# Optimization experiments

Measured on AMD Instinct MI355X. Metric: run time of the kernel, lower is better.

The kernel has to match this reference:

```python
import jax, jax.numpy as jnp
import numpy as np

B, D, N = 8, 512, 4096
HEADS, DH = 8, 64
HID = HEADS * DH  # 512
SCALE = DH ** -0.5


def setup_inputs() -> dict:
    key = jax.random.key(0)
    k0, k1, k2, k3 = jax.random.split(key, 4)
    x = jax.random.normal(k0, (B, D, N), dtype=jnp.float32)
    w_qkv = jax.random.normal(k1, (3 * HID, D), dtype=jnp.float32) * 0.02
    w_out = jax.random.normal(k2, (D, HID), dtype=jnp.float32) * 0.02
    b_out = jax.random.normal(k3, (D,), dtype=jnp.float32) * 0.02
    g = jnp.ones((1, D, 1), dtype=jnp.float32)
    return {"x": x, "w_qkv": w_qkv, "w_out": w_out, "b_out": b_out, "g": g}


def reference(x, w_qkv, w_out, b_out, g):
    # 1x1 Conv1d (no bias) == channel matmul: [b, 3*HID, n]
    qkv = jnp.einsum('od,bdn->bon', w_qkv, x)
    q, k, v = jnp.split(qkv, 3, axis=1)
    # b (h c) n -> b h c n
    q = q.reshape(B, HEADS, DH, N)
    k = k.reshape(B, HEADS, DH, N)
    v = v.reshape(B, HEADS, DH, N)
    q = jax.nn.softmax(q, axis=2) * SCALE  # softmax over feature dim d
    k = jax.nn.softmax(k, axis=3)          # softmax over sequence dim n
    context = jnp.einsum('bhdn,bhen->bhde', k, v)   # [b,h,d,e]
    out = jnp.einsum('bhde,bhdn->bhen', context, q)  # [b,h,e,n]
    out = out.reshape(B, HID, N)
    # 1x1 Conv1d with bias
    y = jnp.einsum('oh,bhn->bon', w_out, out) + b_out[None, :, None]
    # RMSNorm: F.normalize(y, dim=1) * g * sqrt(D)
    norm = jnp.sqrt(jnp.sum(y * y, axis=1, keepdims=True))
    y = y / jnp.maximum(norm, 1e-12) * g * jnp.asarray(D, y.dtype) ** 0.5
    return y
```

## Files before the change

kernel.cpp:

```cpp
#include <hip/hip_runtime.h>
#include <math.h>

#define B 8
#define D 512
#define N 4096
#define HEADS 8
#define DH 64
#define HID 512
#define O3 1536
#define KDIM 512
#define SCALE 0.125f
#define SQRT_D 22.62741699796952f

typedef __attribute__((ext_vector_type(4))) float f32x4;
typedef __attribute__((ext_vector_type(8))) short bf16x8;

static __device__ __forceinline__ unsigned short f2bf(float f) {
    unsigned int u = __float_as_uint(f);
    unsigned int r = (u + 0x7fffu + ((u >> 16) & 1u)) >> 16;
    return (unsigned short)r;
}

static __device__ __forceinline__ float bf2f(unsigned short u) {
    return __uint_as_float((unsigned int)u << 16);
}

static __device__ __forceinline__ void gload_lds16(const void* g, void* l) {
    __builtin_amdgcn_global_load_lds(
        (const __attribute__((address_space(1))) unsigned int*)g,
        (__attribute__((address_space(3))) unsigned int*)l, 16, 0, 0);
}

__global__ __launch_bounds__(256) void prep(const float* __restrict__ x,
                                            unsigned short* __restrict__ xT,
                                            const float* __restrict__ w,
                                            unsigned short* __restrict__ wb) {
    if (blockIdx.z == B) {
        int i = ((blockIdx.y * 96 + blockIdx.x) * 256 + threadIdx.x) * 4;
        float4 v = *(const float4*)(w + i);
        __align__(8) unsigned short o[4] = {f2bf(v.x), f2bf(v.y), f2bf(v.z), f2bf(v.w)};
        *(uint2*)(wb + i) = *(const uint2*)o;
        return;
    }
    if (blockIdx.x >= 64) return;
    __shared__ float tile[64][65];
    const int n0 = blockIdx.x * 64, d0 = blockIdx.y * 64, b = blockIdx.z;
    const float* xb = x + (size_t)b * D * N;
    unsigned short* xTb = xT + (size_t)b * N * KDIM;
    const int t = threadIdx.x;
    const int r = t >> 4, c4 = (t & 15) * 4;
#pragma unroll
    for (int i = 0; i < 4; ++i) {
        int row = r + i * 16;
        float4 v = *(const float4*)(xb + (size_t)(d0 + row) * N + n0 + c4);
        tile[row][c4 + 0] = v.x;
        tile[row][c4 + 1] = v.y;
        tile[row][c4 + 2] = v.z;
        tile[row][c4 + 3] = v.w;
    }
    __syncthreads();
#pragma unroll
    for (int pass = 0; pass < 2; ++pass) {
        int orow = (t >> 3) + pass * 32;
        int oc = (t & 7) * 8;
        __align__(16) unsigned short o[8];
#pragma unroll
        for (int e = 0; e < 8; ++e) o[e] = f2bf(tile[oc + e][orow]);
        *(uint4*)(xTb + (size_t)(n0 + orow) * KDIM + d0 + oc) = *(const uint4*)o;
    }
}

#define STAGE_H(PTR, REGION, TILE0, KT, H)                                         \
    _Pragma("unroll") for (int sub = 0; sub < 2; ++sub)                            \
        gload_lds16(PTR + (size_t)((TILE0) + (H) * 128 + spr[sub]) * KDIM          \
                        + (KT) * 64 + scoff[sub],                                  \
                    lds + (REGION) + ((KT) & 1) * 32768 + (H) * 16384              \
                        + sub * 8192 + t * 16);

#define PHASE_A(MG, KS)                                                            \
    _Pragma("unroll") for (int j = 0; j < 4; ++j)                                  \
        afr[j] = *(const bf16x8*)(lds + rbuf + arb + ((MG) * 4 + j) * 2048 + xa[KS]);

#define PHASE_B(KS)                                                               \
    _Pragma("unroll") for (int nf = 0; nf < 4; ++nf)                               \
        bfr[nf] = *(const bf16x8*)(lds + 65536 + rbuf + brb + nf * 2048 + xa[KS]);

#define PHASE_MMA(MG)                                                              \
    asm volatile("s_waitcnt lgkmcnt(0)" ::: "memory");                             \
    __builtin_amdgcn_sched_barrier(0);                                             \
    __builtin_amdgcn_s_setprio(1);                                                 \
    _Pragma("unroll") for (int j = 0; j < 4; ++j)                                  \
        _Pragma("unroll") for (int nf = 0; nf < 4; ++nf)                           \
            acc[(MG) * 4 + j][nf] = __builtin_amdgcn_mfma_f32_16x16x32_bf16(       \
                afr[j], bfr[nf], acc[(MG) * 4 + j][nf], 0, 0, 0);                  \
    __builtin_amdgcn_s_setprio(0);

#define PBAR __builtin_amdgcn_s_barrier();

#define GEMM256_CORE(A_PTR, BT_PTR)                                                \
    __shared__ __align__(16) char lds[131072];                                     \
    const int t = threadIdx.x;                                                     \
    const int lane = t & 63;                                                       \
    const int wid = t >> 6;                                                        \
    const int wm = wid >> 2, wn = wid & 3;                                         \
    int spr[2], scoff[2];                                                          \
    _Pragma("unroll") for (int sub = 0; sub < 2; ++sub) {                          \
        int p = sub * 8192 + t * 16;                                               \
        spr[sub] = p >> 7;                                                         \
        int spc = (p >> 4) & 7;                                                    \
        scoff[sub] = (spc ^ (spr[sub] & 7)) * 8;                                   \
    }                                                                              \
    int xa[2];                                                                     \
    _Pragma("unroll") for (int ks = 0; ks < 2; ++ks)                               \
        xa[ks] = ((ks * 4 + (lane >> 4)) ^ (lane & 7)) << 4;                       \
    const int arb = (wm * 128 + (lane & 15)) * 128;                                \
    const int brb = (wn * 64 + (lane & 15)) * 128;                                 \
    f32x4 acc[8][4] = {};                                                          \
    bf16x8 afr[4], bfr[4];                                                         \
    STAGE_H(A_PTR, 0, row0, 0, 0)                                                  \
    STAGE_H(A_PTR, 0, row0, 0, 1)                                                  \
    STAGE_H(BT_PTR, 65536, col0, 0, 0)                                             \
    STAGE_H(BT_PTR, 65536, col0, 0, 1)                                             \
    for (int kt = 0; kt < 8; ++kt) {                                               \
        const int rbuf = (kt & 1) * 32768;                                         \
        if (kt < 7) {                                                              \
            STAGE_H(A_PTR, 0, row0, kt + 1, 0)                                     \
            STAGE_H(A_PTR, 0, row0, kt + 1, 1)                                     \
            STAGE_H(BT_PTR, 65536, col0, kt + 1, 0)                                \
            STAGE_H(BT_PTR, 65536, col0, kt + 1, 1)                                \
            asm volatile("s_waitcnt vmcnt(8)" ::: "memory");                       \
        } else {                                                                   \
            asm volatile("s_waitcnt vmcnt(0)" ::: "memory");                       \
        }                                                                          \
        __builtin_amdgcn_s_barrier();                                              \
        __builtin_amdgcn_sched_barrier(0);                                         \
        PHASE_A(0, 0) PHASE_B(0) PHASE_MMA(0) PBAR                                 \
        PHASE_A(1, 0) PHASE_MMA(1) PBAR                                            \
        PHASE_A(0, 1) PHASE_B(1) PHASE_MMA(0) PBAR                                 \
        PHASE_A(1, 1) PHASE_MMA(1) PBAR                                            \
    }

__global__ __launch_bounds__(512, 2) void gemm_qkv(const unsigned short* __restrict__ Aw,
                                                   const unsigned short* __restrict__ BTall,
                                                   unsigned short* __restrict__ qT,
                                                   unsigned short* __restrict__ kvall) {
    const int b = blockIdx.z;
    const unsigned short* A = Aw;
    const unsigned short* BT = BTall + (size_t)b * N * KDIM;
    const int row0 = blockIdx.y * 256;
    const int col0 = blockIdx.x * 256;
    GEMM256_CORE(A, BT)

    const int g = lane >> 4;
    if (blockIdx.y < 2) {
#pragma unroll
        for (int g2 = 0; g2 < 2; ++g2) {
            const int h = blockIdx.y * 4 + wm * 2 + g2;
#pragma unroll
            for (int nf = 0; nf < 4; ++nf) {
                float mx = -1e30f;
#pragma unroll
                for (int j = 0; j < 4; ++j)
#pragma unroll
                    for (int r = 0; r < 4; ++r) mx = fmaxf(mx, acc[g2 * 4 + j][nf][r]);
                mx = fmaxf(mx, __shfl_xor(mx, 16));
                mx = fmaxf(mx, __shfl_xor(mx, 32));
                float e[16];
                float s = 0.f;
#pragma unroll
                for (int j = 0; j < 4; ++j)
#pragma unroll
                    for (int r = 0; r < 4; ++r) {
                        e[j * 4 + r] = __expf(acc[g2 * 4 + j][nf][r] - mx);
                        s += e[j * 4 + r];
                    }
                s += __shfl_xor(s, 16);
                s += __shfl_xor(s, 32);
                float rs = SCALE / s;
                int n = col0 + wn * 64 + nf * 16 + (lane & 15);
                unsigned short* dst = qT + ((size_t)b * N + n) * KDIM + h * 64 + g * 4;
#pragma unroll
                for (int j = 0; j < 4; ++j) {
                    __align__(8) unsigned short o4[4] = {
                        f2bf(e[j * 4 + 0] * rs), f2bf(e[j * 4 + 1] * rs),
                        f2bf(e[j * 4 + 2] * rs), f2bf(e[j * 4 + 3] * rs)};
                    *(uint2*)(dst + j * 16) = *(const uint2*)o4;
                }
            }
        }
    } else {
        unsigned short* C = kvall + (size_t)b * 1024 * N;
        const int rbase = row0 - 512 + wm * 128;
#pragma unroll
        for (int mf = 0; mf < 8; ++mf) {
            int row_b = rbase + mf * 16 + g * 4;
#pragma unroll
            for (int nf = 0; nf < 4; ++nf) {
                int col = col0 + wn * 64 + nf * 16 + (lane & 15);
#pragma unroll
                for (int r = 0; r < 4; ++r)
                    C[(size_t)(row_b + r) * N + col] = f2bf(acc[mf][nf][r]);
            }
        }
    }
}

__global__ __launch_bounds__(256) void context_mfma3(const unsigned short* __restrict__ kvb,
                                                     float* __restrict__ ctx,
                                                     float* __restrict__ ksum) {
    const int ch = blockIdx.x, h = blockIdx.y, b = blockIdx.z;
    const int K0 = ch * 512;
    const unsigned short* kbase = kvb + ((size_t)b * 1024 + h * DH) * (size_t)N + K0;
    const unsigned short* vbase = kvb + ((size_t)b * 1024 + 512 + h * DH) * (size_t)N + K0;

    __shared__ __align__(16) unsigned short Ks[64 * 64];
    __shared__ __align__(16) unsigned short Vs[64 * 64];

    const int t = threadIdx.x;
    const int lane = t & 63;
    const int wv = t >> 6;

    const int kr = t >> 2;
    const int kc = (t & 3) * 16;
    const int kchunk0 = kc >> 3;
    const int kdst0 = kr * 128 + (((kchunk0 + 0) ^ (kr & 7)) << 4);
    const int kdst1 = kr * 128 + (((kchunk0 + 1) ^ (kr & 7)) << 4);

    int vrow[2], vcoff[2];
#pragma unroll
    for (int i = 0; i < 2; ++i) {
        int p = i * 4096 + t * 16;
        int pr = p >> 7;
        int pc = (p >> 4) & 7;
        vrow[i] = pr;
        vcoff[i] = (pc ^ (pr & 7)) * 8;
    }

    const int ar = wv * 16 + (lane & 15);
    int aoff[2], boff[4][2];
#pragma unroll
    for (int s = 0; s < 2; ++s) {
        int chunk = s * 4 + (lane >> 4);
        aoff[s] = ar * 128 + ((chunk ^ (ar & 7)) << 4);
#pragma unroll
        for (int nf = 0; nf < 4; ++nf) {
            int br = nf * 16 + (lane & 15);
            boff[nf][s] = br * 128 + ((chunk ^ (br & 7)) << 4);
        }
    }

    bf16x8 ones;
#pragma unroll
    for (int j = 0; j < 8; ++j) ones[j] = (short)0x3F80;

    f32x4 acc[4] = {};
    f32x4 accs = {};

    for (int k0 = 0; k0 < 512; k0 += 64) {
#pragma unroll
        for (int i = 0; i < 2; ++i)
            gload_lds16(vbase + (size_t)vrow[i] * N + k0 + vcoff[i],
                        (char*)Vs + i * 4096 + t * 16);
        __align__(16) unsigned short raw[16];
        *(uint4*)raw = *(const uint4*)(kbase + (size_t)kr * N + k0 + kc);
        *(uint4*)(raw + 8) = *(const uint4*)(kbase + (size_t)kr * N + k0 + kc + 8);
        __align__(16) unsigned short o[16];
#pragma unroll
        for (int j = 0; j < 16; ++j) o[j] = f2bf(__expf(bf2f(raw[j])));
        *(uint4*)((char*)Ks + kdst0) = *(const uint4*)o;
        *(uint4*)((char*)Ks + kdst1) = *(const uint4*)(o + 8);
        __syncthreads();

        bf16x8 av[2], bv[4][2];
#pragma unroll
        for (int s = 0; s < 2; ++s) {
            av[s] = *(const bf16x8*)((const char*)Ks + aoff[s]);
#pragma unroll
            for (int nf = 0; nf < 4; ++nf)
                bv[nf][s] = *(const bf16x8*)((const char*)Vs + boff[nf][s]);
        }
#pragma unroll
        for (int s = 0; s < 2; ++s) {
#pragma unroll
            for (int nf = 0; nf < 4; ++nf)
                acc[nf] = __builtin_amdgcn_mfma_f32_16x16x32_bf16(av[s], bv[nf][s], acc[nf], 0, 0, 0);
            accs = __builtin_amdgcn_mfma_f32_16x16x32_bf16(av[s], ones, accs, 0, 0, 0);
        }
        __syncthreads();
    }

    float* cbase = ctx + ((size_t)(b * HEADS + h)) * DH * DH;
    const int drow = wv * 16 + (lane >> 4) * 4;
#pragma unroll
    for (int nf = 0; nf < 4; ++nf) {
        int e = nf * 16 + (lane & 15);
#pragma unroll
        for (int rr = 0; rr < 4; ++rr)
            atomicAdd(&cbase[(drow + rr) * DH + e], acc[nf][rr]);
    }
    if ((lane & 15) == 0) {
#pragma unroll
        for (int rr = 0; rr < 4; ++rr)
            atomicAdd(&ksum[b * 512 + h * DH + drow + rr], accs[rr]);
    }
}

__global__ __launch_bounds__(256) void fold_wout3(const float* __restrict__ w_out,
                                                  const float* __restrict__ ctx,
                                                  const float* __restrict__ ksum,
                                                  unsigned short* __restrict__ w2) {
    const int ot = blockIdx.x, h = blockIdx.y, b = blockIdx.z;
    __shared__ __align__(16) unsigned short As[128 * 64];
    __shared__ __align__(16) unsigned short Bs[64 * 64];
    const int t = threadIdx.x;
    const int lane = t & 63;
    const int wv = t >> 6;

#pragma unroll
    for (int i = 0; i < 8; ++i) {
        int lin = t + i * 256;
        int r = lin >> 4;
        int c4 = (lin & 15) * 4;
        float4 v = *(const float4*)(w_out + (size_t)(ot * 128 + r) * HID + h * 64 + c4);
        __align__(8) unsigned short o4[4] = {f2bf(v.x), f2bf(v.y), f2bf(v.z), f2bf(v.w)};
        int chunk = c4 >> 3;
        int off = (c4 & 7) * 2;
        *(uint2*)((char*)As + r * 128 + ((chunk ^ (r & 7)) << 4) + off) = *(const uint2*)o4;
    }
    const float* cb = ctx + ((size_t)(b * HEADS + h)) * DH * DH;
    const float* ks = ksum + b * 512 + h * 64;
#pragma unroll
    for (int i = 0; i < 4; ++i) {
        int lin = t + i * 256;
        int r = lin >> 4;
        int c4 = (lin & 15) * 4;
        float inv = 1.0f / ks[r];
        float4 v = *(const float4*)(cb + (size_t)r * DH + c4);
        __align__(8) unsigned short o4[4] = {f2bf(v.x * inv), f2bf(v.y * inv),
                                             f2bf(v.z * inv), f2bf(v.w * inv)};
        int chunk = c4 >> 3;
        int off = (c4 & 7) * 2;
        *(uint2*)((char*)Bs + r * 128 + ((chunk ^ (r & 7)) << 4) + off) = *(const uint2*)o4;
    }
    __syncthreads();

    f32x4 acc[2][4] = {};
#pragma unroll
    for (int s = 0; s < 2; ++s) {
        int chunk = s * 4 + (lane >> 4);
        bf16x8 bf[4];
#pragma unroll
        for (int nf = 0; nf < 4; ++nf) {
            int brow = nf * 16 + (lane & 15);
            bf[nf] = *(const bf16x8*)((const char*)Bs + brow * 128 + ((chunk ^ (brow & 7)) << 4));
        }
#pragma unroll
        for (int mm = 0; mm < 2; ++mm) {
            int arow = (wv * 2 + mm) * 16 + (lane & 15);
            bf16x8 a = *(const bf16x8*)((const char*)As + arow * 128 + ((chunk ^ (arow & 7)) << 4));
#pragma unroll
            for (int nf = 0; nf < 4; ++nf)
                acc[mm][nf] = __builtin_amdgcn_mfma_f32_16x16x32_bf16(a, bf[nf], acc[mm][nf], 0, 0, 0);
        }
    }

#pragma unroll
    for (int mm = 0; mm < 2; ++mm) {
        int o_base = ot * 128 + (wv * 2 + mm) * 16 + (lane >> 4) * 4;
#pragma unroll
        for (int nf = 0; nf < 4; ++nf) {
            int d = nf * 16 + (lane & 15);
#pragma unroll
            for (int rr = 0; rr < 4; ++rr)
                w2[((size_t)(b * D) + o_base + rr) * D + h * 64 + d] = f2bf(acc[mm][nf][rr]);
        }
    }
}

__global__ __launch_bounds__(512, 2) void gemm_y(const unsigned short* __restrict__ w2all,
                                                 const unsigned short* __restrict__ qTall,
                                                 const float* __restrict__ bias,
                                                 float* __restrict__ yall,
                                                 float* __restrict__ colsum) {
    const int b = blockIdx.z;
    const unsigned short* A = w2all + (size_t)b * D * D;
    const unsigned short* BT = qTall + (size_t)b * N * KDIM;
    float* y = yall + (size_t)b * D * N;
    const int row0 = blockIdx.y * 256;
    const int col0 = blockIdx.x * 256;
    GEMM256_CORE(A, BT)

    const int g = lane >> 4;
    float csum[4] = {0.f, 0.f, 0.f, 0.f};
#pragma unroll
    for (int mf = 0; mf < 8; ++mf) {
        int row_b = row0 + wm * 128 + mf * 16 + g * 4;
#pragma unroll
        for (int r = 0; r < 4; ++r) {
            float bv = bias[row_b + r];
#pragma unroll
            for (int nf = 0; nf < 4; ++nf) {
                int col = col0 + wn * 64 + nf * 16 + (lane & 15);
                float e = acc[mf][nf][r] + bv;
                y[(size_t)(row_b + r) * N + col] = e;
                csum[nf] += e * e;
            }
        }
    }
#pragma unroll
    for (int nf = 0; nf < 4; ++nf) {
        csum[nf] += __shfl_xor(csum[nf], 16);
        csum[nf] += __shfl_xor(csum[nf], 32);
    }
    if ((lane & 48) == 0) {
#pragma unroll
        for (int nf = 0; nf < 4; ++nf) {
            int col = col0 + wn * 64 + nf * 16 + (lane & 15);
            atomicAdd(&colsum[b * N + col], csum[nf]);
        }
    }
}

__global__ __launch_bounds__(256) void rmsnorm5(float4* __restrict__ y,
                                                const float4* __restrict__ colsum,
                                                const float* __restrict__ g) {
    const size_t total = (size_t)B * D * N / 4;
    for (size_t i = blockIdx.x * 256 + threadIdx.x; i < total; i += 524288) {
        int b = (int)(i >> 19);
        int rem = (int)(i & 524287);
        int o = rem >> 10;
        int n4 = rem & 1023;
        float4 v = y[i];
        float4 cs = colsum[b * 1024 + n4];
        float go = g[o];
        float r0 = SQRT_D / fmaxf(sqrtf(cs.x), 1e-12f);
        float r1 = SQRT_D / fmaxf(sqrtf(cs.y), 1e-12f);
        float r2 = SQRT_D / fmaxf(sqrtf(cs.z), 1e-12f);
        float r3 = SQRT_D / fmaxf(sqrtf(cs.w), 1e-12f);
        v.x *= r0 * go;
        v.y *= r1 * go;
        v.z *= r2 * go;
        v.w *= r3 * go;
        y[i] = v;
    }
}

extern "C" void kernel_launch(void* const* d_in, const int* in_sizes, int n_in,
                              void* d_out, int out_size, void* d_ws, size_t ws_size,
                              hipStream_t stream) {
    const float* x = (const float*)d_in[0];
    const float* w_qkv = (const float*)d_in[1];
    const float* w_out = (const float*)d_in[2];
    const float* b_out = (const float*)d_in[3];
    const float* g = (const float*)d_in[4];
    float* out = (float*)d_out;

    unsigned short* kvb = (unsigned short*)d_ws;
    float* ctx = (float*)(kvb + (size_t)B * 1024 * N);
    float* ksum = ctx + (size_t)B * HEADS * DH * DH;
    float* colsum = ksum + B * 512;
    unsigned short* w2 = (unsigned short*)(colsum + B * N);
    unsigned short* wqb = w2 + (size_t)B * D * D;
    unsigned short* xT = wqb + (size_t)O3 * KDIM;
    unsigned short* qT = xT + (size_t)B * N * KDIM;

    hipMemsetAsync(ctx, 0,
                   ((size_t)B * HEADS * DH * DH + B * 512 + B * N) * sizeof(float), stream);

    prep<<<dim3(96, 8, B + 1), 256, 0, stream>>>(x, xT, w_qkv, wqb);

    gemm_qkv<<<dim3(N / 256, O3 / 256, B), 512, 0, stream>>>(wqb, xT, qT, kvb);

    context_mfma3<<<dim3(8, HEADS, B), 256, 0, stream>>>(kvb, ctx, ksum);
    fold_wout3<<<dim3(4, HEADS, B), 256, 0, stream>>>(w_out, ctx, ksum, w2);

    gemm_y<<<dim3(N / 256, D / 256, B), 512, 0, stream>>>(w2, qT, b_out, out, colsum);

    rmsnorm5<<<dim3(2048), 256, 0, stream>>>((float4*)out, (const float4*)colsum, g);
}
```

Measured before the change: 169.5 us.

## Fuse RMSNorm into output GEMM with full-channel tiles and trim GEMM barriers

Replaces the output GEMM plus separate RMSNorm pass with one kernel whose block covers all 512 output channels for 64 columns. The column norm is reduced in LDS and applied before the single store. This removes the y write/read round trip, the colsum atomics, the colsum memset and one launch. It also drops the per-phase barriers in the shared 256x256 GEMM core in favour of one extra barrier at the top of each k-step. The cost is 144KB of LDS per block, so only one block fits per CU, and re-staging the full A matrix for every 64-column tile.

Result: faster. 145.8 us (median of 3 runs) (-13.9%).

```diff
diff --git a/kernel.cpp b/kernel.cpp
--- a/kernel.cpp
+++ b/kernel.cpp
@@ -94,8 +94,6 @@
             acc[(MG) * 4 + j][nf] = __builtin_amdgcn_mfma_f32_16x16x32_bf16(       \
                 afr[j], bfr[nf], acc[(MG) * 4 + j][nf], 0, 0, 0);                  \
     __builtin_amdgcn_s_setprio(0);
-
-#define PBAR __builtin_amdgcn_s_barrier();
 
 #define GEMM256_CORE(A_PTR, BT_PTR)                                                \
     __shared__ __align__(16) char lds[131072];                                     \
@@ -123,6 +121,7 @@
     STAGE_H(BT_PTR, 65536, col0, 0, 1)                                             \
     for (int kt = 0; kt < 8; ++kt) {                                               \
         const int rbuf = (kt & 1) * 32768;                                         \
+        __builtin_amdgcn_s_barrier();                                              \
         if (kt < 7) {                                                              \
             STAGE_H(A_PTR, 0, row0, kt + 1, 0)                                     \
             STAGE_H(A_PTR, 0, row0, kt + 1, 1)                                     \
@@ -134,10 +133,10 @@
         }                                                                          \
         __builtin_amdgcn_s_barrier();                                              \
         __builtin_amdgcn_sched_barrier(0);                                         \
-        PHASE_A(0, 0) PHASE_B(0) PHASE_MMA(0) PBAR                                 \
-        PHASE_A(1, 0) PHASE_MMA(1) PBAR                                            \
-        PHASE_A(0, 1) PHASE_B(1) PHASE_MMA(0) PBAR                                 \
-        PHASE_A(1, 1) PHASE_MMA(1) PBAR                                            \
+        PHASE_A(0, 0) PHASE_B(0) PHASE_MMA(0)                                      \
+        PHASE_A(1, 0) PHASE_MMA(1)                                                 \
+        PHASE_A(0, 1) PHASE_B(1) PHASE_MMA(0)                                      \
+        PHASE_A(1, 1) PHASE_MMA(1)                                                 \
     }
 
 __global__ __launch_bounds__(512, 2) void gemm_qkv(const unsigned short* __restrict__ Aw,
@@ -377,33 +376,87 @@
     }
 }
 
-__global__ __launch_bounds__(512, 2) void gemm_y(const unsigned short* __restrict__ w2all,
-                                                 const unsigned short* __restrict__ qTall,
-                                                 const float* __restrict__ bias,
-                                                 float* __restrict__ yall,
-                                                 float* __restrict__ colsum) {
+#define YSTAGE(KT)                                                                 \
+    _Pragma("unroll") for (int sub = 0; sub < 8; ++sub)                            \
+        gload_lds16(A + (size_t)(sub * 64 + srow) * KDIM + (KT) * 64 + sco,        \
+                    lds + ((KT) & 1) * 65536 + sub * 8192 + t * 16);               \
+    gload_lds16(BT + (size_t)(col0 + srow) * KDIM + (KT) * 64 + sco,               \
+                lds + 131072 + ((KT) & 1) * 8192 + t * 16);
+
+__global__ __launch_bounds__(512, 1) void gemm_y_fused(const unsigned short* __restrict__ w2all,
+                                                       const unsigned short* __restrict__ qTall,
+                                                       const float* __restrict__ bias,
+                                                       const float* __restrict__ g,
+                                                       float* __restrict__ outall) {
     const int b = blockIdx.z;
     const unsigned short* A = w2all + (size_t)b * D * D;
     const unsigned short* BT = qTall + (size_t)b * N * KDIM;
-    float* y = yall + (size_t)b * D * N;
-    const int row0 = blockIdx.y * 256;
-    const int col0 = blockIdx.x * 256;
-    GEMM256_CORE(A, BT)
-
-    const int g = lane >> 4;
+    float* out = outall + (size_t)b * D * N;
+    const int col0 = blockIdx.x * 64;
+
+    __shared__ __align__(16) char lds[147456];
+    const int t = threadIdx.x;
+    const int lane = t & 63;
+    const int wid = t >> 6;
+
+    const int srow = t >> 3;
+    const int sco = ((t & 7) ^ (srow & 7)) * 8;
+
+    int xa[2];
+#pragma unroll
+    for (int ks = 0; ks < 2; ++ks)
+        xa[ks] = ((ks * 4 + (lane >> 4)) ^ (lane & 7)) << 4;
+    const int arb = (wid * 64 + (lane & 15)) * 128;
+    const int brb = (lane & 15) * 128;
+
+    f32x4 acc[4][4] = {};
+    bf16x8 afr[4], bfr[4];
+
+    YSTAGE(0)
+    for (int kt = 0; kt < 8; ++kt) {
+        const int abuf = (kt & 1) * 65536;
+        const int bbuf = 131072 + (kt & 1) * 8192;
+        __builtin_amdgcn_s_barrier();
+        if (kt < 7) {
+            YSTAGE(kt + 1)
+            asm volatile("s_waitcnt vmcnt(9)" ::: "memory");
+        } else {
+            asm volatile("s_waitcnt vmcnt(0)" ::: "memory");
+        }
+        __builtin_amdgcn_s_barrier();
+        __builtin_amdgcn_sched_barrier(0);
+#pragma unroll
+        for (int ks = 0; ks < 2; ++ks) {
+#pragma unroll
+            for (int mf = 0; mf < 4; ++mf)
+                afr[mf] = *(const bf16x8*)(lds + abuf + arb + mf * 2048 + xa[ks]);
+#pragma unroll
+            for (int nf = 0; nf < 4; ++nf)
+                bfr[nf] = *(const bf16x8*)(lds + bbuf + brb + nf * 2048 + xa[ks]);
+            asm volatile("s_waitcnt lgkmcnt(0)" ::: "memory");
+            __builtin_amdgcn_sched_barrier(0);
+            __builtin_amdgcn_s_setprio(1);
+#pragma unroll
+            for (int mf = 0; mf < 4; ++mf)
+#pragma unroll
+                for (int nf = 0; nf < 4; ++nf)
+                    acc[mf][nf] = __builtin_amdgcn_mfma_f32_16x16x32_bf16(
+                        afr[mf], bfr[nf], acc[mf][nf], 0, 0, 0);
+            __builtin_amdgcn_s_setprio(0);
+        }
+    }
+
     float csum[4] = {0.f, 0.f, 0.f, 0.f};
 #pragma unroll
-    for (int mf = 0; mf < 8; ++mf) {
-        int row_b = row0 + wm * 128 + mf * 16 + g * 4;
+    for (int mf = 0; mf < 4; ++mf) {
+        int row = wid * 64 + mf * 16 + (lane >> 4) * 4;
 #pragma unroll
         for (int r = 0; r < 4; ++r) {
-            float bv = bias[row_b + r];
+            float bv = bias[row + r];
 #pragma unroll
             for (int nf = 0; nf < 4; ++nf) {
-                int col = col0 + wn * 64 + nf * 16 + (lane & 15);
-                float e = acc[mf][nf][r] + bv;
-                y[(size_t)(row_b + r) * N + col] = e;
-                csum[nf] += e * e;
+                acc[mf][nf][r] += bv;
+                csum[nf] += acc[mf][nf][r] * acc[mf][nf][r];
             }
         }
     }
@@ -412,36 +465,34 @@
         csum[nf] += __shfl_xor(csum[nf], 16);
         csum[nf] += __shfl_xor(csum[nf], 32);
     }
-    if ((lane & 48) == 0) {
-#pragma unroll
-        for (int nf = 0; nf < 4; ++nf) {
-            int col = col0 + wn * 64 + nf * 16 + (lane & 15);
-            atomicAdd(&colsum[b * N + col], csum[nf]);
-        }
-    }
-}
-
-__global__ __launch_bounds__(256) void rmsnorm5(float4* __restrict__ y,
-                                                const float4* __restrict__ colsum,
-                                                const float* __restrict__ g) {
-    const size_t total = (size_t)B * D * N / 4;
-    for (size_t i = blockIdx.x * 256 + threadIdx.x; i < total; i += 524288) {
-        int b = (int)(i >> 19);
-        int rem = (int)(i & 524287);
-        int o = rem >> 10;
-        int n4 = rem & 1023;
-        float4 v = y[i];
-        float4 cs = colsum[b * 1024 + n4];
-        float go = g[o];
-        float r0 = SQRT_D / fmaxf(sqrtf(cs.x), 1e-12f);
-        float r1 = SQRT_D / fmaxf(sqrtf(cs.y), 1e-12f);
-        float r2 = SQRT_D / fmaxf(sqrtf(cs.z), 1e-12f);
-        float r3 = SQRT_D / fmaxf(sqrtf(cs.w), 1e-12f);
-        v.x *= r0 * go;
-        v.y *= r1 * go;
-        v.z *= r2 * go;
-        v.w *= r3 * go;
-        y[i] = v;
+    __syncthreads();
+    float* scr = (float*)lds;
+    if (lane < 16) {
+#pragma unroll
+        for (int nf = 0; nf < 4; ++nf) scr[wid * 64 + nf * 16 + lane] = csum[nf];
+    }
+    __syncthreads();
+    float rinv[4];
+#pragma unroll
+    for (int nf = 0; nf < 4; ++nf) {
+        int c = nf * 16 + (lane & 15);
+        float s = 0.f;
+#pragma unroll
+        for (int w = 0; w < 8; ++w) s += scr[w * 64 + c];
+        rinv[nf] = SQRT_D / fmaxf(sqrtf(s), 1e-12f);
+    }
+#pragma unroll
+    for (int mf = 0; mf < 4; ++mf) {
+        int row = wid * 64 + mf * 16 + (lane >> 4) * 4;
+#pragma unroll
+        for (int r = 0; r < 4; ++r) {
+            float gv = g[row + r];
+#pragma unroll
+            for (int nf = 0; nf < 4; ++nf) {
+                int col = col0 + nf * 16 + (lane & 15);
+                out[(size_t)(row + r) * N + col] = acc[mf][nf][r] * rinv[nf] * gv;
+            }
+        }
     }
 }
 
@@ -458,14 +509,12 @@
     unsigned short* kvb = (unsigned short*)d_ws;
     float* ctx = (float*)(kvb + (size_t)B * 1024 * N);
     float* ksum = ctx + (size_t)B * HEADS * DH * DH;
-    float* colsum = ksum + B * 512;
-    unsigned short* w2 = (unsigned short*)(colsum + B * N);
+    unsigned short* w2 = (unsigned short*)(ksum + B * 512);
     unsigned short* wqb = w2 + (size_t)B * D * D;
     unsigned short* xT = wqb + (size_t)O3 * KDIM;
     unsigned short* qT = xT + (size_t)B * N * KDIM;
 
-    hipMemsetAsync(ctx, 0,
-                   ((size_t)B * HEADS * DH * DH + B * 512 + B * N) * sizeof(float), stream);
+    hipMemsetAsync(ctx, 0, ((size_t)B * HEADS * DH * DH + B * 512) * sizeof(float), stream);
 
     prep<<<dim3(96, 8, B + 1), 256, 0, stream>>>(x, xT, w_qkv, wqb);
 
@@ -474,7 +523,5 @@
     context_mfma3<<<dim3(8, HEADS, B), 256, 0, stream>>>(kvb, ctx, ksum);
     fold_wout3<<<dim3(4, HEADS, B), 256, 0, stream>>>(w_out, ctx, ksum, w2);
 
-    gemm_y<<<dim3(N / 256, D / 256, B), 512, 0, stream>>>(w2, qT, b_out, out, colsum);
-
-    rmsnorm5<<<dim3(2048), 256, 0, stream>>>((float4*)out, (const float4*)colsum, g);
-}
+    gemm_y_fused<<<dim3(N / 64, 1, B), 512, 0, stream>>>(w2, qT, b_out, g, out);
+}
```
